# Kernel tuning notes

Hardware: AMD Instinct MI355X
Metric: run time of the kernel (lower is better)

Reference implementation:

```python
import jax, jax.numpy as jnp
import numpy as np

BETA = 0.9
THRESHOLD = 1.0
NUM_STEPS = 100

# Heaviside spike with snntorch-default ATan surrogate gradient (alpha=2):
# forward: 1[u > 0]; backward: g / (1 + (pi*u)^2)
@jax.custom_vjp
def spike(u):
    return (u > 0).astype(u.dtype)

def _spike_fwd(u):
    return (u > 0).astype(u.dtype), u

def _spike_bwd(u, g):
    return (g / (1.0 + (jnp.pi * u) ** 2),)

spike.defvjp(_spike_fwd, _spike_bwd)


def setup_inputs() -> dict:
    key = jax.random.key(0)
    ks = jax.random.split(key, 8)
    B, D_IN, H, D_OUT = 256, 1024, 2048, 1024
    def lin(k, fan_out, fan_in):
        bound = 1.0 / np.sqrt(fan_in)
        kw, kb = jax.random.split(k)
        W = jax.random.uniform(kw, (fan_out, fan_in), jnp.float32, -bound, bound)
        b = jax.random.uniform(kb, (fan_out,), jnp.float32, -bound, bound)
        return W, b
    W0, b0 = lin(ks[0], H, D_IN)
    W1, b1 = lin(ks[1], H, H)
    W2, b2 = lin(ks[2], D_OUT, H)
    x = jax.random.normal(ks[3], (B, D_IN), jnp.float32)
    return {"x": x, "W0": W0, "b0": b0, "W1": W1, "b1": b1, "W2": W2, "b2": b2}


def _lif(cur, mem_prev):
    # snntorch Leaky, reset_mechanism='subtract': reset computed from previous
    # state (detached), then mem update, then fire.
    reset = jax.lax.stop_gradient((mem_prev > THRESHOLD).astype(cur.dtype))
    mem_new = BETA * mem_prev + cur - reset * THRESHOLD
    spk = spike(mem_new - THRESHOLD)
    # NOTE: the source module does `mem[i], spk[i] = layer(cur, mem[i])` while
    # snn.Leaky returns (spk, mem) -- i.e. the outputs are SWAPPED. We reproduce
    # that faithfully: the stored 'mem' state is the spike, and the stored 'spk'
    # (fed to the next layer / emitted as output) is the membrane potential.
    return spk, mem_new


def reference(x, W0, b0, W1, b1, W2, b2):
    B = x.shape[0]
    m_init = (jnp.zeros((B, W0.shape[0]), x.dtype),
              jnp.zeros((B, W1.shape[0]), x.dtype),
              jnp.zeros((B, W2.shape[0]), x.dtype))

    cur0 = x @ W0.T + b0  # input is constant across steps; hoist the GEMM

    def step(mems, _):
        m0_spk, s0_mem = _lif(cur0, mems[0])
        cur1 = s0_mem @ W1.T + b1          # 'spk[0]' in source is actually mem
        m1_spk, s1_mem = _lif(cur1, mems[1])
        cur2 = s1_mem @ W2.T + b2          # 'spk[-2]' = layer-1 'spk' (= mem)
        m2_spk, s2_mem = _lif(cur2, mems[2])
        return (m0_spk, m1_spk, m2_spk), s2_mem

    _, outs = jax.lax.scan(step, m_init, None, length=NUM_STEPS)
    return outs  # [num_steps, batch, output_size]
```

## Files before the change

kernel.cpp:

```cpp
#include <hip/hip_runtime.h>


typedef unsigned short ushort_t;
typedef __attribute__((ext_vector_type(8))) short bf16x8;
typedef __attribute__((ext_vector_type(4))) float f32x4;

#define SDELTA 1.0e-3f
#define NS 12

__device__ inline ushort_t f2bf(float f) {
    unsigned u = __float_as_uint(f);
    u += 0x7FFFu + ((u >> 16) & 1u);
    return (ushort_t)(u >> 16);
}
__device__ inline float bf2f(ushort_t h) { return __uint_as_float((unsigned)h << 16); }
__device__ inline float4 ld4(const float* p) { return *reinterpret_cast<const float4*>(p); }

__device__ inline void gload16(const void* g, void* l) {
    __builtin_amdgcn_global_load_lds(
        (__attribute__((address_space(1))) void*)g,
        (__attribute__((address_space(3))) void*)l, 16, 0, 0);
}

__device__ inline void do_split(const float4* src, ushort_t* dst, int i, int logK)
{
    float4 v = src[i];
    const int K = 1 << logK;
    const int e0 = i * 4;
    const int r = e0 >> logK, k = e0 & (K - 1);
    ushort_t* row = dst + (size_t)r * 2 * K;
    ushort4 h, l;
    h.x = f2bf(v.x); l.x = f2bf(v.x - bf2f(h.x));
    h.y = f2bf(v.y); l.y = f2bf(v.y - bf2f(h.y));
    h.z = f2bf(v.z); l.z = f2bf(v.z - bf2f(h.z));
    h.w = f2bf(v.w); l.w = f2bf(v.w - bf2f(h.w));
    *reinterpret_cast<ushort4*>(row + k) = h;
    *reinterpret_cast<ushort4*>(row + K + k) = l;
}

__device__ __attribute__((always_inline)) inline void gemm_body(
    const ushort_t* __restrict__ A, const ushort_t* __restrict__ W,
    float* __restrict__ P, int M, int N, int K, int Kc, int nx, int ny,
    int lin, int nwg, ushort_t* As, ushort_t* Ws)
{
    const int swzb = (lin & 7) * (nwg >> 3) + (lin >> 3);
    const int nxy = nx * ny;
    const int bz  = swzb / nxy;
    const int rem = swzb - bz * nxy;
    const int by  = rem / nx;
    const int bx  = rem - by * nx;

    const int tid  = threadIdx.x;
    const int lane = tid & 63;
    const int wid  = tid >> 6;
    const int row0 = by * 128;
    const int col0 = bx * 128;
    const int k0   = bz * Kc;
    const int st   = 2 * K;
    const int aoff = (k0 < K) ? k0 : (k0 - K);
    const int woff = (k0 < 2 * K) ? k0 : (k0 - 2 * K);

    const int srow = wid * 32 + (lane >> 3);
    const int scol = (((lane & 7) ^ ((lane >> 3) & 7))) * 8;
    const ushort_t* Ag = A + (size_t)(row0 + srow) * st + aoff + scol;
    const ushort_t* Wg = W + (size_t)(col0 + srow) * st + woff + scol;

    const int wr = wid >> 1, wc = wid & 1;
    const int l15 = lane & 15;
    const int kh  = lane >> 4;
    const int swz8 = l15 & 7;
    const int ch0 = ((kh + 0) ^ swz8) * 8;
    const int ch1 = ((kh + 4) ^ swz8) * 8;
    int aRow[4], bRow[4];
#pragma unroll
    for (int m = 0; m < 4; ++m) aRow[m] = (wr * 64 + m * 16 + l15) * 64;
#pragma unroll
    for (int n = 0; n < 4; ++n) bRow[n] = (wc * 64 + n * 16 + l15) * 64;

    f32x4 acc[4][4] = {};
    const int NIT = Kc / 64;

    for (int it = 0; it < NIT; ++it) {
        const int kk = it * 64;
#pragma unroll
        for (int i = 0; i < 4; ++i) {
            gload16(Ag + (size_t)(i * 8) * st + kk, &As[(wid * 32 + i * 8) * 64]);
            gload16(Wg + (size_t)(i * 8) * st + kk, &Ws[(wid * 32 + i * 8) * 64]);
        }
        __syncthreads();
#pragma unroll
        for (int ks = 0; ks < 2; ++ks) {
            const int ch = ks ? ch1 : ch0;
            bf16x8 af[4], bf[4];
#pragma unroll
            for (int m = 0; m < 4; ++m)
                af[m] = *reinterpret_cast<const bf16x8*>(&As[aRow[m] + ch]);
#pragma unroll
            for (int n = 0; n < 4; ++n)
                bf[n] = *reinterpret_cast<const bf16x8*>(&Ws[bRow[n] + ch]);
#pragma unroll
            for (int m = 0; m < 4; ++m)
#pragma unroll
                for (int n = 0; n < 4; ++n)
                    acc[m][n] = __builtin_amdgcn_mfma_f32_16x16x32_bf16(
                        af[m], bf[n], acc[m][n], 0, 0, 0);
        }
        __syncthreads();
    }

    float* Pp = P + ((size_t)bz * M + row0) * N + col0;
#pragma unroll
    for (int n = 0; n < 4; ++n) {
        const int col = wc * 64 + n * 16 + l15;
#pragma unroll
        for (int m = 0; m < 4; ++m) {
            const int rb = wr * 64 + m * 16 + kh * 4;
#pragma unroll
            for (int i = 0; i < 4; ++i)
                Pp[(size_t)(rb + i) * N + col] = acc[m][n][i];
        }
    }
}

__global__ __launch_bounds__(256) void gemm_splitk(
    const ushort_t* __restrict__ A, const ushort_t* __restrict__ W,
    float* __restrict__ P, int M, int N, int K, int Kc, int nx, int ny)
{
    __shared__ ushort_t As[128 * 64];
    __shared__ ushort_t Ws[128 * 64];
    gemm_body(A, W, P, M, N, K, Kc, nx, ny, blockIdx.x, gridDim.x, As, Ws);
}

__global__ __launch_bounds__(256) void gemm0_cvt12(
    const ushort_t* __restrict__ xb, const ushort_t* __restrict__ Wb0,
    float* __restrict__ P,
    const float4* __restrict__ W1, const float4* __restrict__ W2,
    ushort_t* __restrict__ Wb1, ushort_t* __restrict__ Wb2)
{
    __shared__ ushort_t As[128 * 64];
    __shared__ ushort_t Ws[128 * 64];
    const int b = blockIdx.x;
    if (b < 384) {
        gemm_body(xb, Wb0, P, 256, 2048, 1024, 256, 16, 2, b, 384, As, Ws);
    } else if (b < 384 + 4096) {
        do_split(W1, Wb1, (b - 384) * 256 + threadIdx.x, 11);
    } else {
        do_split(W2, Wb2, (b - 4480) * 256 + threadIdx.x, 11);
    }
}

__global__ __launch_bounds__(256) void cvt_xw0(
    const float4* __restrict__ x, const float4* __restrict__ W0,
    ushort_t* __restrict__ xb, ushort_t* __restrict__ Wb0)
{
    const int b = blockIdx.x, tid = threadIdx.x;
    if (b < 256) do_split(x,  xb,  b * 256 + tid, 10);
    else         do_split(W0, Wb0, (b - 256) * 256 + tid, 10);
}

__device__ inline int flag4(float4 v, int e0, int* loc, int lc)
{
    float vv[4] = {v.x, v.y, v.z, v.w};
#pragma unroll
    for (int c = 0; c < 4; ++c)
        if ((fabsf(vv[c] - 1.0f) < SDELTA) || (fabsf(vv[c] - 0.1f) < SDELTA))
            loc[lc++] = e0 + c;
    return lc;
}

__device__ inline void wsplit2(ushort_t* row, int k, float4 v)
{
    ushort4 h, l;
    h.x = f2bf(v.x); l.x = f2bf(v.x - bf2f(h.x));
    h.y = f2bf(v.y); l.y = f2bf(v.y - bf2f(h.y));
    h.z = f2bf(v.z); l.z = f2bf(v.z - bf2f(h.z));
    h.w = f2bf(v.w); l.w = f2bf(v.w - bf2f(h.w));
    *reinterpret_cast<ushort4*>(row + k) = h;
    *reinterpret_cast<ushort4*>(row + 2048 + k) = l;
}

__device__ inline void patch2(ushort_t* row, int c, float v)
{
    ushort_t h = f2bf(v);
    ushort_t l = f2bf(v - bf2f(h));
    row[c] = h; row[2048 + c] = l;
}

__device__ inline float4 lifstep(float4 cur, float4 gate)
{
    float4 o;
    o.x = cur.x + ((gate.x > 1.0f) ? 0.9f : 0.0f);
    o.y = cur.y + ((gate.y > 1.0f) ? 0.9f : 0.0f);
    o.z = cur.z + ((gate.z > 1.0f) ? 0.9f : 0.0f);
    o.w = cur.w + ((gate.w > 1.0f) ? 0.9f : 0.0f);
    return o;
}

__device__ inline double wred(double p)
{
#pragma unroll
    for (int off = 32; off; off >>= 1) p += __shfl_down(p, off);
    return __shfl(p, 0);
}

__global__ __launch_bounds__(256) void fused0(
    const float4* __restrict__ P, const float* __restrict__ bias,
    float* __restrict__ C0f, ushort_t* __restrict__ A1b,
    const float* __restrict__ X, const float* __restrict__ W0,
    const float* __restrict__ b0f)
{
    __shared__ int flist[1024];
    __shared__ int fcnt;
    if (threadIdx.x == 0) fcnt = 0;
    __syncthreads();

    const int i = blockIdx.x * 256 + threadIdx.x;
    float4 s = P[i];
#pragma unroll
    for (int j = 1; j < NS; ++j) {
        float4 t = P[(size_t)j * 131072 + i];
        s.x += t.x; s.y += t.y; s.z += t.z; s.w += t.w;
    }
    const float4 bv = *reinterpret_cast<const float4*>(bias + ((i * 4) & 2047));
    s.x += bv.x; s.y += bv.y; s.z += bv.z; s.w += bv.w;
    reinterpret_cast<float4*>(C0f)[i] = s;
    int loc[4];
    int lc = flag4(s, i * 4, loc, 0);
    for (int j = 0; j < lc; ++j) { int p = atomicAdd(&fcnt, 1); flist[p] = loc[j]; }
    float4 mi = lifstep(s, s);
    const int e0 = i * 4, r = e0 >> 11, k = e0 & 2047;
    wsplit2(A1b + (size_t)r * 4096, k, s);
    wsplit2(A1b + (size_t)(256 + r) * 4096, k, mi);
    __syncthreads();

    const int lane = threadIdx.x & 63;
    const int wid  = threadIdx.x >> 6;
    for (int e = wid; e < fcnt; e += 4) {
        const int idx = flist[e];
        const int rr = idx >> 11, cc = idx & 2047;
        double p = 0.0;
        for (int kk = lane * 4; kk < 1024; kk += 256) {
            float4 a4 = ld4(X + (size_t)rr * 1024 + kk);
            float4 w4 = ld4(W0 + (size_t)cc * 1024 + kk);
            p = fma((double)a4.x, (double)w4.x, p);
            p = fma((double)a4.y, (double)w4.y, p);
            p = fma((double)a4.z, (double)w4.z, p);
            p = fma((double)a4.w, (double)w4.w, p);
        }
        const double tot = wred(p);
        if (lane == 0) {
            float c = (float)(tot + (double)b0f[cc]);
            C0f[idx] = c;
            float mi2 = c + ((c > 1.0f) ? 0.9f : 0.0f);
            patch2(A1b + (size_t)rr * 4096, cc, c);
            patch2(A1b + (size_t)(256 + rr) * 4096, cc, mi2);
        }
    }
}

__global__ __launch_bounds__(256) void fused1(
    const float4* __restrict__ P, const float* __restrict__ bias,
    float* __restrict__ C1f, ushort_t* __restrict__ A2b,
    const float* __restrict__ C0, const float* __restrict__ W1)
{
    __shared__ int flist[2048];
    __shared__ int fcnt;
    if (threadIdx.x == 0) fcnt = 0;
    __syncthreads();

    const int i = blockIdx.x * 256 + threadIdx.x;
    float4* C1 = reinterpret_cast<float4*>(C1f);
    float4 c0 = P[i];
    float4 ci = P[131072 + i];
#pragma unroll
    for (int j = 1; j < NS; ++j) {
        float4 t0 = P[(size_t)j * 262144 + i];
        float4 t1 = P[(size_t)j * 262144 + 131072 + i];
        c0.x += t0.x; c0.y += t0.y; c0.z += t0.z; c0.w += t0.w;
        ci.x += t1.x; ci.y += t1.y; ci.z += t1.z; ci.w += t1.w;
    }
    const float4 bv = *reinterpret_cast<const float4*>(bias + ((i * 4) & 2047));
    c0.x += bv.x; c0.y += bv.y; c0.z += bv.z; c0.w += bv.w;
    ci.x += bv.x; ci.y += bv.y; ci.z += bv.z; ci.w += bv.w;
    C1[i] = c0;
    C1[131072 + i] = ci;
    int loc[8];
    int lc = flag4(c0, i * 4, loc, 0);
    lc = flag4(ci, (131072 + i) * 4, loc, lc);
    for (int j = 0; j < lc; ++j) { int p = atomicAdd(&fcnt, 1); flist[p] = loc[j]; }
    float4 m1 = lifstep(ci, c0);
    float4 m2 = lifstep(ci, m1);
    const int e0 = i * 4, r = e0 >> 11, k = e0 & 2047;
    wsplit2(A2b + (size_t)r * 4096, k, c0);
    wsplit2(A2b + (size_t)(256 + r) * 4096, k, m1);
    wsplit2(A2b + (size_t)(512 + r) * 4096, k, m2);
    __syncthreads();

    const int lane = threadIdx.x & 63;
    const int wid  = threadIdx.x >> 6;
    for (int e = wid; e < fcnt; e += 4) {
        const int idx = flist[e];
        const int cc = idx & 2047;
        const int rp = (idx >> 11) & 255;
        double p0 = 0.0, p1 = 0.0;
        for (int kk = lane * 4; kk < 2048; kk += 256) {
            float4 a4 = ld4(C0 + (size_t)rp * 2048 + kk);
            float4 w4 = ld4(W1 + (size_t)cc * 2048 + kk);
            float4 b4 = lifstep(a4, a4);
            p0 = fma((double)a4.x, (double)w4.x, p0);
            p0 = fma((double)a4.y, (double)w4.y, p0);
            p0 = fma((double)a4.z, (double)w4.z, p0);
            p0 = fma((double)a4.w, (double)w4.w, p0);
            p1 = fma((double)b4.x, (double)w4.x, p1);
            p1 = fma((double)b4.y, (double)w4.y, p1);
            p1 = fma((double)b4.z, (double)w4.z, p1);
            p1 = fma((double)b4.w, (double)w4.w, p1);
        }
        const double t0 = wred(p0);
        const double t1 = wred(p1);
        if (lane == 0) {
            float fc0 = (float)(t0 + (double)bias[cc]);
            float fci = (float)(t1 + (double)bias[cc]);
            C1f[(size_t)rp * 2048 + cc] = fc0;
            C1f[(size_t)(256 + rp) * 2048 + cc] = fci;
            float m1s = fci + ((fc0 > 1.0f) ? 0.9f : 0.0f);
            float m2s = fci + ((m1s > 1.0f) ? 0.9f : 0.0f);
            patch2(A2b + (size_t)rp * 4096, cc, fc0);
            patch2(A2b + (size_t)(256 + rp) * 4096, cc, m1s);
            patch2(A2b + (size_t)(512 + rp) * 4096, cc, m2s);
        }
    }
}

__global__ __launch_bounds__(256) void fused2(
    const float4* __restrict__ P, const float* __restrict__ bias,
    float* __restrict__ C2f, const float* __restrict__ C1,
    const float* __restrict__ W2)
{
    __shared__ int flist[3072];
    __shared__ int fcnt;
    if (threadIdx.x == 0) fcnt = 0;
    __syncthreads();

    const int i = blockIdx.x * 256 + threadIdx.x;
    float4* C2 = reinterpret_cast<float4*>(C2f);
    const float4 bv = *reinterpret_cast<const float4*>(bias + ((i * 4) & 1023));
#pragma unroll
    for (int v = 0; v < 3; ++v) {
        float4 s = P[(size_t)v * 65536 + i];
#pragma unroll
        for (int j = 1; j < NS; ++j) {
            float4 t = P[(size_t)j * 196608 + (size_t)v * 65536 + i];
            s.x += t.x; s.y += t.y; s.z += t.z; s.w += t.w;
        }
        s.x += bv.x; s.y += bv.y; s.z += bv.z; s.w += bv.w;
        C2[(size_t)v * 65536 + i] = s;
        int loc[4];
        int lc = flag4(s, (v * 65536 + i) * 4, loc, 0);
        for (int j = 0; j < lc; ++j) { int p = atomicAdd(&fcnt, 1); flist[p] = loc[j]; }
    }
    __syncthreads();

    const int lane = threadIdx.x & 63;
    const int wid  = threadIdx.x >> 6;
    for (int e = wid; e < fcnt; e += 4) {
        const int idx = flist[e];
        const int cc = idx & 1023;
        const int rp = (idx >> 10) & 255;
        double pA = 0.0, pB = 0.0, pC = 0.0;
        for (int kk = lane * 4; kk < 2048; kk += 256) {
            float4 c04 = ld4(C1 + (size_t)rp * 2048 + kk);
            float4 ci4 = ld4(C1 + (size_t)(256 + rp) * 2048 + kk);
            float4 w4  = ld4(W2 + (size_t)cc * 2048 + kk);
            float4 m14 = lifstep(ci4, c04);
            float4 m24 = lifstep(ci4, m14);
            pA = fma((double)c04.x, (double)w4.x, pA);
            pA = fma((double)c04.y, (double)w4.y, pA);
            pA = fma((double)c04.z, (double)w4.z, pA);
            pA = fma((double)c04.w, (double)w4.w, pA);
            pB = fma((double)m14.x, (double)w4.x, pB);
            pB = fma((double)m14.y, (double)w4.y, pB);
            pB = fma((double)m14.z, (double)w4.z, pB);
            pB = fma((double)m14.w, (double)w4.w, pB);
            pC = fma((double)m24.x, (double)w4.x, pC);
            pC = fma((double)m24.y, (double)w4.y, pC);
            pC = fma((double)m24.z, (double)w4.z, pC);
            pC = fma((double)m24.w, (double)w4.w, pC);
        }
        const double tA = wred(pA);
        const double tB = wred(pB);
        const double tC = wred(pC);
        if (lane == 0) {
            C2f[(size_t)rp * 1024 + cc]         = (float)(tA + (double)bias[cc]);
            C2f[(size_t)(256 + rp) * 1024 + cc] = (float)(tB + (double)bias[cc]);
            C2f[(size_t)(512 + rp) * 1024 + cc] = (float)(tC + (double)bias[cc]);
        }
    }
}

__global__ __launch_bounds__(256) void lif2_bcast(const float4* __restrict__ c2,
                                                  float4* __restrict__ out, int n4)
{
    int i = blockIdx.x * 256 + threadIdx.x;
    if (i >= n4) return;
    float4 c0 = c2[i], c1 = c2[n4 + i], ci = c2[2 * n4 + i];
    float4 m0 = c0;
    float4 m1 = lifstep(c1, m0);
    float4 m2 = lifstep(ci, m1);
    float4 m3 = lifstep(ci, m2);
    int t0 = blockIdx.y * 4;
#pragma unroll
    for (int j = 0; j < 4; ++j) {
        int t = t0 + j;
        float4 v = (t == 0) ? m0 : (t == 1) ? m1 : (t == 2) ? m2 : m3;
        out[(size_t)t * n4 + i] = v;
    }
}

extern "C" void kernel_launch(void* const* d_in, const int* in_sizes, int n_in,
                              void* d_out, int out_size, void* d_ws, size_t ws_size,
                              hipStream_t stream)
{
    const float* x  = (const float*)d_in[0];
    const float* W0 = (const float*)d_in[1];
    const float* b0 = (const float*)d_in[2];
    const float* W1 = (const float*)d_in[3];
    const float* b1 = (const float*)d_in[4];
    const float* W2 = (const float*)d_in[5];
    const float* b2 = (const float*)d_in[6];
    float* out = (float*)d_out;
    float* ws  = (float*)d_ws;

    float* C0 = ws;
    float* C1 = ws + 524288;
    float* C2 = ws + 1572864;

    ushort_t* Wb0 = (ushort_t*)(out);
    ushort_t* Wb1 = (ushort_t*)(out + 2097152);
    ushort_t* Wb2 = (ushort_t*)(out + 6291456);
    ushort_t* xb  = (ushort_t*)(out + 8388608);
    ushort_t* A1b = (ushort_t*)(out + 8650752);
    ushort_t* A2b = (ushort_t*)(out + 9699328);
    float* Pbuf   = out + 11272192;

    dim3 blk(256);

    cvt_xw0<<<dim3(2304), blk, 0, stream>>>((const float4*)x, (const float4*)W0,
                                            xb, Wb0);

    gemm0_cvt12<<<dim3(6528), blk, 0, stream>>>(xb, Wb0, Pbuf,
                                                (const float4*)W1, (const float4*)W2,
                                                Wb1, Wb2);
    fused0<<<dim3(512), blk, 0, stream>>>((const float4*)Pbuf, b0, C0,
                                          A1b, x, W0, b0);

    gemm_splitk<<<dim3(768), blk, 0, stream>>>(A1b, Wb1, Pbuf, 512, 2048, 2048, 512, 16, 4);
    fused1<<<dim3(512), blk, 0, stream>>>((const float4*)Pbuf, b1, C1,
                                          A2b, C0, W1);

    gemm_splitk<<<dim3(576), blk, 0, stream>>>(A2b, Wb2, Pbuf, 768, 1024, 2048, 512, 8, 6);
    fused2<<<dim3(256), blk, 0, stream>>>((const float4*)Pbuf, b2, C2, C1, W2);

    lif2_bcast<<<dim3(256, 25), blk, 0, stream>>>((const float4*)C2, (float4*)out, 65536);
}
```

Measured before the change: 145.7 us.

## Fuse LIF broadcast into layer-2 reduction and halve layer-2 split-K factor

The layer-2 split-K GEMM now uses 6 partitions of length 1024 instead of 12 of length 512, so it launches fewer blocks and the reduction reads fewer partial sums. The partials go to a separate buffer placed in the output region for timesteps 80 and later. The former reduction kernel now also computes the LIF states and writes output timesteps 0–79 itself. A small tail kernel writes timesteps 80–99 after the partials there have been consumed. This removes the standalone broadcast launch and the extra reread of C2, at the cost of long per-thread store loops in only 256 blocks and a longer K loop per GEMM block.

```diff
diff --git a/kernel.cpp b/kernel.cpp
--- a/kernel.cpp
+++ b/kernel.cpp
@@ -7,6 +7,7 @@
 
 #define SDELTA 1.0e-3f
 #define NS 12
+#define NS2 6
 
 __device__ inline ushort_t f2bf(float f) {
     unsigned u = __float_as_uint(f);
@@ -332,10 +333,10 @@
     }
 }
 
-__global__ __launch_bounds__(256) void fused2(
+__global__ __launch_bounds__(256) void fused2_bcast(
     const float4* __restrict__ P, const float* __restrict__ bias,
     float* __restrict__ C2f, const float* __restrict__ C1,
-    const float* __restrict__ W2)
+    const float* __restrict__ W2, float4* __restrict__ out)
 {
     __shared__ int flist[3072];
     __shared__ int fcnt;
@@ -349,7 +350,7 @@
     for (int v = 0; v < 3; ++v) {
         float4 s = P[(size_t)v * 65536 + i];
 #pragma unroll
-        for (int j = 1; j < NS; ++j) {
+        for (int j = 1; j < NS2; ++j) {
             float4 t = P[(size_t)j * 196608 + (size_t)v * 65536 + i];
             s.x += t.x; s.y += t.y; s.z += t.z; s.w += t.w;
         }
@@ -396,25 +397,34 @@
             C2f[(size_t)(512 + rp) * 1024 + cc] = (float)(tC + (double)bias[cc]);
         }
     }
-}
-
-__global__ __launch_bounds__(256) void lif2_bcast(const float4* __restrict__ c2,
-                                                  float4* __restrict__ out, int n4)
-{
-    int i = blockIdx.x * 256 + threadIdx.x;
-    if (i >= n4) return;
-    float4 c0 = c2[i], c1 = c2[n4 + i], ci = c2[2 * n4 + i];
+    __syncthreads();
+
+    float4 c0 = C2[i];
+    float4 c1 = C2[65536 + i];
+    float4 ci = C2[131072 + i];
     float4 m0 = c0;
     float4 m1 = lifstep(c1, m0);
     float4 m2 = lifstep(ci, m1);
     float4 m3 = lifstep(ci, m2);
-    int t0 = blockIdx.y * 4;
-#pragma unroll
-    for (int j = 0; j < 4; ++j) {
-        int t = t0 + j;
-        float4 v = (t == 0) ? m0 : (t == 1) ? m1 : (t == 2) ? m2 : m3;
-        out[(size_t)t * n4 + i] = v;
-    }
+    out[i] = m0;
+    out[65536 + i] = m1;
+    out[131072 + i] = m2;
+    for (int t = 3; t < 80; ++t)
+        out[(size_t)t * 65536 + i] = m3;
+}
+
+__global__ __launch_bounds__(256) void tail_bcast(const float4* __restrict__ c2,
+                                                  float4* __restrict__ out)
+{
+    const int i = blockIdx.x * 256 + threadIdx.x;
+    float4 c0 = c2[i], c1 = c2[65536 + i], ci = c2[131072 + i];
+    float4 m1 = lifstep(c1, c0);
+    float4 m2 = lifstep(ci, m1);
+    float4 m3 = lifstep(ci, m2);
+    const int t0 = 80 + blockIdx.y * 4;
+#pragma unroll
+    for (int j = 0; j < 4; ++j)
+        out[(size_t)(t0 + j) * 65536 + i] = m3;
 }
 
 extern "C" void kernel_launch(void* const* d_in, const int* in_sizes, int n_in,
@@ -442,6 +452,7 @@
     ushort_t* A1b = (ushort_t*)(out + 8650752);
     ushort_t* A2b = (ushort_t*)(out + 9699328);
     float* Pbuf   = out + 11272192;
+    float* Pbuf2  = out + 20971520;
 
     dim3 blk(256);
 
@@ -458,8 +469,8 @@
     fused1<<<dim3(512), blk, 0, stream>>>((const float4*)Pbuf, b1, C1,
                                           A2b, C0, W1);
 
-    gemm_splitk<<<dim3(576), blk, 0, stream>>>(A2b, Wb2, Pbuf, 768, 1024, 2048, 512, 8, 6);
-    fused2<<<dim3(256), blk, 0, stream>>>((const float4*)Pbuf, b2, C2, C1, W2);
-
-    lif2_bcast<<<dim3(256, 25), blk, 0, stream>>>((const float4*)C2, (float4*)out, 65536);
-}
+    gemm_splitk<<<dim3(288), blk, 0, stream>>>(A2b, Wb2, Pbuf2, 768, 1024, 2048, 1024, 8, 6);
+    fused2_bcast<<<dim3(256), blk, 0, stream>>>((const float4*)Pbuf2, b2, C2, C1, W2,
+                                                (float4*)out);
+    tail_bcast<<<dim3(256, 5), blk, 0, stream>>>((const float4*)C2, (float4*)out);
+}
```

After: 142.8 us. Within noise of the previous version (-1.9%).
